# Optimization experiments

Hardware: AMD Instinct MI355X
Metric: run time of the kernel (lower is better)

## Reference

```python
import jax, jax.numpy as jnp
import numpy as np

T, D, E, K = 8192, 7168, 256, 8
G, LG = 8, 4  # n_expert_groups, n_limited_groups
ROUTE_SCALE = 2.5


def setup_inputs() -> dict:
    key = jax.random.key(0)
    k1, k2, k3 = jax.random.split(key, 3)
    x = jax.random.normal(k1, (T, D), dtype=jnp.float32)
    W = jax.random.normal(k2, (E, D), dtype=jnp.float32) * (1.0 / np.sqrt(D))
    bias = jax.random.normal(k3, (E,), dtype=jnp.float32) * 0.01
    return {"x": x, "W": W, "bias": bias}


def reference(x, W, bias):
    # linear scorer: [T, E]
    logits = jnp.einsum("td,ed->te", x, W)
    original_scores = jax.nn.sigmoid(logits)
    scores = original_scores + bias  # bias only affects routing, not weights

    # group selection: reshape [T, G, E//G]; group score = sum of top-2 (bias path)
    scores_g = scores.reshape(T, G, E // G)
    group_scores = jax.lax.top_k(scores_g, 2)[0].sum(axis=-1)  # [T, G]
    _, gidx = jax.lax.top_k(group_scores, LG)  # [T, LG]
    keep = jnp.any(jnp.arange(G)[None, None, :] == gidx[:, :, None], axis=1)  # [T, G]
    scores_masked = jnp.where(keep[:, :, None], scores_g, -jnp.inf).reshape(T, E)

    # final top-k experts
    _, indices = jax.lax.top_k(scores_masked, K)  # [T, K] int32
    weights = jnp.take_along_axis(original_scores, indices, axis=1)  # [T, K]
    weights = weights / weights.sum(axis=-1, keepdims=True)  # sigmoid normalization
    weights = weights * ROUTE_SCALE
    weights = weights.astype(x.dtype)

    # per-expert token counts (indices unique per row, so scatter(1)+sum == histogram)
    counts = jnp.zeros((E,), dtype=jnp.int32).at[indices.reshape(-1)].add(1)
    return weights, indices.astype(jnp.int64), counts
```

## Files before the change

kernel.cpp:

```cpp
#include <hip/hip_runtime.h>
#include <math.h>
#include <stdint.h>

#define T_TOK 8192
#define D_DIM 7168
#define E_EXP 256
#define K_SEL 8
#define G_GRP 8
#define LG_GRP 4
#define ROUTE_SCALE 2.5f

#define BM 64
#define BN 128
#define BK 64
#define NKT (D_DIM / BK)
#define KT_HALF (NKT / 2)
#define SCALE_LO 2048.0f
#define INV_SCALE (1.0f / 2048.0f)

typedef _Float16 half_t;
typedef _Float16 half8 __attribute__((ext_vector_type(8)));
typedef float f32x4 __attribute__((ext_vector_type(4)));

#define WF_HALVES_PER_H (2 * 112 * 16 * 512)

__device__ __forceinline__ void load_lds16(const void* g, void* l) {
    __builtin_amdgcn_global_load_lds(
        (const __attribute__((address_space(1))) uint32_t*)g,
        (__attribute__((address_space(3))) uint32_t*)l, 16, 0, 0);
}

__global__ __launch_bounds__(256)
void convert_W_kernel(const float* __restrict__ W, half_t* __restrict__ Wf) {
    const int u = blockIdx.x * 256 + threadIdx.x;
    const int slot = u & 63;
    const int ks   = (u >> 6) & 1;
    const int p    = (u >> 7) & 7;
    const int t2   = u >> 10;
    const int kt   = t2 % 112;
    const int nb   = t2 / 112;
    const int e = nb * 128 + p * 16 + (slot & 15);
    const int k = kt * 64 + ks * 32 + (slot >> 4) * 8;

    const float* src = W + (size_t)e * D_DIM + k;
    float4 v0 = *(const float4*)src;
    float4 v1 = *(const float4*)(src + 4);
    float f[8] = {v0.x, v0.y, v0.z, v0.w, v1.x, v1.y, v1.z, v1.w};
    half8 hi, lo;
    #pragma unroll
    for (int j = 0; j < 8; j++) {
        const half_t h = (half_t)f[j];
        hi[j] = h;
        lo[j] = (half_t)((f[j] - (float)h) * SCALE_LO);
    }
    *(half8*)&Wf[(size_t)u * 8] = hi;
    *(half8*)&Wf[(size_t)WF_HALVES_PER_H + (size_t)u * 8] = lo;
}

__global__ __launch_bounds__(256, 2)
void gemm_logits_f16split(const float* __restrict__ x,
                          const half_t* __restrict__ Wf,
                          float* __restrict__ plane0,
                          float* __restrict__ plane1) {
    __shared__ __align__(16) half_t Ah[4 * 2 * 64 * 8];
    __shared__ __align__(16) half_t Al[4 * 2 * 64 * 8];
    __shared__ __align__(16) half_t Bbuf[2][32][512];

    const int tid = threadIdx.x;
    const int bid = blockIdx.x;
    const int nb    = bid & 1;
    const int split = (bid >> 1) & 1;
    const int m_blk = bid >> 2;
    const int row0 = m_blk * BM;
    const int ks0  = split * KT_HALF;

    const float* __restrict__ xA = x + (size_t)row0 * D_DIM;
    float* __restrict__ plane = split ? plane1 : plane0;

    const int wave = tid >> 6, lane = tid & 63;
    const int q = lane >> 4;
    const int mp0 = (wave >> 1) * 2;
    const int np0 = (wave & 1) * 4;

    float4 pa[2][2];

    auto load_A = [&](int kt) {
        const int kbase = kt * BK;
        #pragma unroll
        for (int i = 0; i < 2; i++) {
            const int u = i * 256 + tid;
            const int r = u >> 3, k8 = u & 7;
            const float* p = xA + (size_t)r * D_DIM + kbase + k8 * 8;
            pa[i][0] = *(const float4*)p;
            pa[i][1] = *(const float4*)(p + 4);
        }
    };

    auto stage_A = [&]() {
        #pragma unroll
        for (int i = 0; i < 2; i++) {
            const int u = i * 256 + tid;
            const int r = u >> 3, k8 = u & 7;
            float f[8] = {pa[i][0].x, pa[i][0].y, pa[i][0].z, pa[i][0].w,
                          pa[i][1].x, pa[i][1].y, pa[i][1].z, pa[i][1].w};
            half8 hi, lo;
            #pragma unroll
            for (int j = 0; j < 8; j++) {
                const half_t h = (half_t)f[j];
                hi[j] = h;
                lo[j] = (half_t)((f[j] - (float)h) * SCALE_LO);
            }
            const int m = r & 15, qq = k8 & 3, kss = k8 >> 2;
            const int slot = (m + 16 * qq) ^ k8;
            const int off = (((r >> 4) * 2 + kss) * 64 + slot) * 8;
            *(half8*)&Ah[off] = hi;
            *(half8*)&Al[off] = lo;
        }
    };

    auto issue_B = [&](int tt) {
        const int kt = ks0 + tt;
        half_t* bb = &Bbuf[tt & 1][0][0];
        #pragma unroll
        for (int i = 0; i < 8; i++) {
            const int s32 = i * 4 + wave;
            const int h = s32 >> 4, sl = s32 & 15;
            const half_t* src = Wf +
                ((size_t)((h * 2 + nb) * 112 + kt) * 16 + sl) * 512 + lane * 8;
            load_lds16(src, bb + s32 * 512);
        }
    };

    f32x4 ach[2][4] = {}, acc[2][4] = {};

    auto compute = [&](int tt) {
        const half_t* bb = &Bbuf[tt & 1][0][0];
        #pragma unroll
        for (int ks = 0; ks < 2; ks++) {
            const int slot = lane ^ ((ks << 2) | q);
            half8 ah[2], al[2], bh[4], bl[4];
            #pragma unroll
            for (int mi = 0; mi < 2; mi++) {
                const int off = (((mp0 + mi) * 2 + ks) * 64 + slot) * 8;
                ah[mi] = *(const half8*)&Ah[off];
                al[mi] = *(const half8*)&Al[off];
            }
            #pragma unroll
            for (int ni = 0; ni < 4; ni++) {
                const int s32 = (np0 + ni) * 2 + ks;
                bh[ni] = *(const half8*)&bb[s32 * 512 + lane * 8];
                bl[ni] = *(const half8*)&bb[(16 + s32) * 512 + lane * 8];
            }
            #pragma unroll
            for (int mi = 0; mi < 2; mi++)
                #pragma unroll
                for (int ni = 0; ni < 4; ni++) {
                    ach[mi][ni] = __builtin_amdgcn_mfma_f32_16x16x32_f16(ah[mi], bh[ni], ach[mi][ni], 0, 0, 0);
                    acc[mi][ni] = __builtin_amdgcn_mfma_f32_16x16x32_f16(ah[mi], bl[ni], acc[mi][ni], 0, 0, 0);
                    acc[mi][ni] = __builtin_amdgcn_mfma_f32_16x16x32_f16(al[mi], bh[ni], acc[mi][ni], 0, 0, 0);
                }
        }
    };

    issue_B(0);
    load_A(ks0);

    #pragma unroll 1
    for (int tt = 0; tt < KT_HALF; tt++) {
        __syncthreads();
        stage_A();
        __syncthreads();
        if (tt + 1 < KT_HALF) {
            issue_B(tt + 1);
            load_A(ks0 + tt + 1);
        }
        compute(tt);
    }

    const int col0 = nb * BN;
    #pragma unroll
    for (int mi = 0; mi < 2; mi++)
        #pragma unroll
        for (int ni = 0; ni < 4; ni++) {
            const f32x4 vh = ach[mi][ni];
            const f32x4 vc = acc[mi][ni];
            const int ex = col0 + (np0 + ni) * 16 + (lane & 15);
            #pragma unroll
            for (int r = 0; r < 4; r++) {
                const int tok = row0 + (mp0 + mi) * 16 + q * 4 + r;
                plane[(size_t)tok * E_EXP + ex] = vh[r] + vc[r] * INV_SCALE;
            }
        }
}

__global__ __launch_bounds__(256)
void routing_kernel(const float* __restrict__ plane0,
                    const float* __restrict__ plane1,
                    const float* __restrict__ bias,
                    float* __restrict__ out_w,
                    float* __restrict__ out_i) {
    const int wave = threadIdx.x >> 6;
    const int lane = threadIdx.x & 63;
    const int t    = blockIdx.x * 4 + wave;

    const float4 l0 = *(const float4*)(plane0 + (size_t)t * E_EXP + lane * 4);
    const float4 l1 = *(const float4*)(plane1 + (size_t)t * E_EXP + lane * 4);
    const float4 bi = *(const float4*)(bias + lane * 4);
    float lg[4] = {l0.x + l1.x, l0.y + l1.y, l0.z + l1.z, l0.w + l1.w};

    float orig[4], s[4];
    #pragma unroll
    for (int j = 0; j < 4; j++)
        orig[j] = 1.0f / (1.0f + expf(-lg[j]));
    s[0] = orig[0] + bi.x; s[1] = orig[1] + bi.y;
    s[2] = orig[2] + bi.z; s[3] = orig[3] + bi.w;

    float p1 = fmaxf(s[0], s[1]), p2 = fminf(s[0], s[1]);
    float q1 = fmaxf(s[2], s[3]), q2 = fminf(s[2], s[3]);
    float m1 = fmaxf(p1, q1);
    float m2 = fmaxf(fminf(p1, q1), (p1 >= q1) ? p2 : q2);

    #pragma unroll
    for (int off = 1; off <= 4; off <<= 1) {
        float o1 = __shfl_xor(m1, off);
        float o2 = __shfl_xor(m2, off);
        float M1 = fmaxf(m1, o1);
        float M2 = fmaxf(fminf(m1, o1), (m1 >= o1) ? m2 : o2);
        m1 = M1; m2 = M2;
    }
    const float gscore = m1 + m2;

    const int g = lane >> 3;
    int cnt = 0;
    #pragma unroll
    for (int j = 0; j < G_GRP; j++) {
        float gj = __shfl(gscore, j * 8);
        cnt += (gj > gscore || (gj == gscore && j < g)) ? 1 : 0;
    }
    const bool keep = (cnt < LG_GRP);

    float smask[4];
    #pragma unroll
    for (int j = 0; j < 4; j++) smask[j] = keep ? s[j] : -INFINITY;

    float wsum = 0.0f, my_o = 0.0f;
    int my_i = 0;

    #pragma unroll
    for (int k = 0; k < K_SEL; k++) {
        float bv = smask[0]; float bo = orig[0]; int bs = 0;
        if (smask[1] > bv) { bv = smask[1]; bo = orig[1]; bs = 1; }
        if (smask[2] > bv) { bv = smask[2]; bo = orig[2]; bs = 2; }
        if (smask[3] > bv) { bv = smask[3]; bo = orig[3]; bs = 3; }
        int bidx = lane * 4 + bs;

        #pragma unroll
        for (int off = 32; off >= 1; off >>= 1) {
            float ov = __shfl_xor(bv, off);
            float oo = __shfl_xor(bo, off);
            int   oi = __shfl_xor(bidx, off);
            if (ov > bv || (ov == bv && oi < bidx)) { bv = ov; bo = oo; bidx = oi; }
        }
        wsum += bo;
        if (lane == k) { my_o = bo; my_i = bidx; }
        if ((bidx >> 2) == lane) {
            const int sl = bidx & 3;
            smask[0] = (sl == 0) ? -INFINITY : smask[0];
            smask[1] = (sl == 1) ? -INFINITY : smask[1];
            smask[2] = (sl == 2) ? -INFINITY : smask[2];
            smask[3] = (sl == 3) ? -INFINITY : smask[3];
        }
    }

    if (lane < K_SEL) {
        out_w[(size_t)t * K_SEL + lane] = my_o * ROUTE_SCALE / wsum;
        out_i[(size_t)t * K_SEL + lane] = (float)my_i;
    }
}

__global__ __launch_bounds__(256)
void count_kernel(const float* __restrict__ idxf, float* __restrict__ out_c) {
    const float fe = (float)blockIdx.x;
    int c = 0;
    const float4* p = (const float4*)idxf;
    for (int i = threadIdx.x; i < (T_TOK * K_SEL / 4); i += 256) {
        float4 v = p[i];
        c += (v.x == fe) + (v.y == fe) + (v.z == fe) + (v.w == fe);
    }
    __shared__ int red[4];
    #pragma unroll
    for (int off = 32; off >= 1; off >>= 1) c += __shfl_down(c, off);
    if ((threadIdx.x & 63) == 0) red[threadIdx.x >> 6] = c;
    __syncthreads();
    if (threadIdx.x == 0)
        out_c[blockIdx.x] = (float)(red[0] + red[1] + red[2] + red[3]);
}

extern "C" void kernel_launch(void* const* d_in, const int* in_sizes, int n_in,
                              void* d_out, int out_size, void* d_ws, size_t ws_size,
                              hipStream_t stream) {
    const float* x    = (const float*)d_in[0];
    const float* W    = (const float*)d_in[1];
    const float* bias = (const float*)d_in[2];

    float* out   = (float*)d_out;
    float* out_w = out;
    float* out_i = out + (size_t)T_TOK * K_SEL;
    float* out_c = out + (size_t)2 * T_TOK * K_SEL;

    float* plane0 = (float*)d_ws;
    float* plane1 = plane0 + (size_t)T_TOK * E_EXP;
    half_t* Wf    = (half_t*)(plane1 + (size_t)T_TOK * E_EXP);

    hipLaunchKernelGGL(convert_W_kernel, dim3(896), dim3(256), 0, stream, W, Wf);
    hipLaunchKernelGGL(gemm_logits_f16split, dim3(512), dim3(256), 0, stream,
                       x, Wf, plane0, plane1);
    hipLaunchKernelGGL(routing_kernel, dim3(T_TOK / 4), dim3(256), 0, stream,
                       plane0, plane1, bias, out_w, out_i);
    hipLaunchKernelGGL(count_kernel, dim3(E_EXP), dim3(256), 0, stream,
                       out_i, out_c);
}
```

Before: 394.3 us.

## Stage fp32 x tiles directly to LDS via async loads and convert in compute loop

Reworks the logits GEMM. M tile grows from 64 to 128 rows, K step shrinks to 32, and split-K goes from 2 to 4 slices, keeping 512 blocks. A tiles are now copied as raw fp32 straight into LDS with global_load_lds, and the fp16 hi/lo split happens in registers during compute. This removes the register staging pass and one barrier per iteration. The costs are redundant A conversion across the two N-column blocks, double the split-K partial planes for the routing kernel to sum, and more accumulators per wave, which adds register pressure.

```diff
diff --git a/kernel.cpp b/kernel.cpp
--- a/kernel.cpp
+++ b/kernel.cpp
@@ -10,19 +10,16 @@
 #define LG_GRP 4
 #define ROUTE_SCALE 2.5f
 
-#define BM 64
-#define BN 128
-#define BK 64
-#define NKT (D_DIM / BK)
-#define KT_HALF (NKT / 2)
+#define BKT 32
+#define NKT32 (D_DIM / BKT)
+#define SPLITK 4
+#define KT_SLICE (NKT32 / SPLITK)
 #define SCALE_LO 2048.0f
 #define INV_SCALE (1.0f / 2048.0f)
 
 typedef _Float16 half_t;
 typedef _Float16 half8 __attribute__((ext_vector_type(8)));
 typedef float f32x4 __attribute__((ext_vector_type(4)));
-
-#define WF_HALVES_PER_H (2 * 112 * 16 * 512)
 
 __device__ __forceinline__ void load_lds16(const void* g, void* l) {
     __builtin_amdgcn_global_load_lds(
@@ -32,15 +29,14 @@
 
 __global__ __launch_bounds__(256)
 void convert_W_kernel(const float* __restrict__ W, half_t* __restrict__ Wf) {
-    const int u = blockIdx.x * 256 + threadIdx.x;
-    const int slot = u & 63;
-    const int ks   = (u >> 6) & 1;
-    const int p    = (u >> 7) & 7;
-    const int t2   = u >> 10;
-    const int kt   = t2 % 112;
-    const int nb   = t2 / 112;
-    const int e = nb * 128 + p * 16 + (slot & 15);
-    const int k = kt * 64 + ks * 32 + (slot >> 4) * 8;
+    const int v = blockIdx.x * 256 + threadIdx.x;
+    const int slot = v & 63;
+    const int p    = (v >> 6) & 7;
+    const int rest = v >> 9;
+    const int ktg  = rest % NKT32;
+    const int n    = rest / NKT32;
+    const int e = n * 128 + p * 16 + (slot & 15);
+    const int k = ktg * BKT + (slot >> 4) * 8;
 
     const float* src = W + (size_t)e * D_DIM + k;
     float4 v0 = *(const float4*)src;
@@ -53,149 +49,112 @@
         hi[j] = h;
         lo[j] = (half_t)((f[j] - (float)h) * SCALE_LO);
     }
-    *(half8*)&Wf[(size_t)u * 8] = hi;
-    *(half8*)&Wf[(size_t)WF_HALVES_PER_H + (size_t)u * 8] = lo;
+    half_t* tile = Wf + ((size_t)(n * NKT32 + ktg)) * 8192;
+    *(half8*)&tile[(p * 2 + 0) * 512 + slot * 8] = hi;
+    *(half8*)&tile[(p * 2 + 1) * 512 + slot * 8] = lo;
 }
 
 __global__ __launch_bounds__(256, 2)
 void gemm_logits_f16split(const float* __restrict__ x,
                           const half_t* __restrict__ Wf,
-                          float* __restrict__ plane0,
-                          float* __restrict__ plane1) {
-    __shared__ __align__(16) half_t Ah[4 * 2 * 64 * 8];
-    __shared__ __align__(16) half_t Al[4 * 2 * 64 * 8];
-    __shared__ __align__(16) half_t Bbuf[2][32][512];
+                          float* __restrict__ planes) {
+    __shared__ __align__(16) float  Abuf[2][4096];
+    __shared__ __align__(16) half_t Bbuf[2][8192];
 
     const int tid = threadIdx.x;
     const int bid = blockIdx.x;
-    const int nb    = bid & 1;
-    const int split = (bid >> 1) & 1;
-    const int m_blk = bid >> 2;
-    const int row0 = m_blk * BM;
-    const int ks0  = split * KT_HALF;
+    const int n    = bid & 1;
+    const int sp   = (bid >> 1) & 3;
+    const int mb   = bid >> 3;
+    const int row0 = mb * 128;
+    const int kt0  = sp * KT_SLICE;
 
     const float* __restrict__ xA = x + (size_t)row0 * D_DIM;
-    float* __restrict__ plane = split ? plane1 : plane0;
+    float* __restrict__ plane = planes + (size_t)sp * T_TOK * E_EXP;
 
     const int wave = tid >> 6, lane = tid & 63;
+    const int wm = wave >> 1, wn = wave & 1;
+    const int np0 = wn * 4;
     const int q = lane >> 4;
-    const int mp0 = (wave >> 1) * 2;
-    const int np0 = (wave & 1) * 4;
-
-    float4 pa[2][2];
-
-    auto load_A = [&](int kt) {
-        const int kbase = kt * BK;
-        #pragma unroll
-        for (int i = 0; i < 2; i++) {
-            const int u = i * 256 + tid;
-            const int r = u >> 3, k8 = u & 7;
-            const float* p = xA + (size_t)r * D_DIM + kbase + k8 * 8;
-            pa[i][0] = *(const float4*)p;
-            pa[i][1] = *(const float4*)(p + 4);
+
+    auto issue = [&](int t) {
+        const int ktg = kt0 + t;
+        const int b = t & 1;
+        #pragma unroll
+        for (int i = 0; i < 4; i++) {
+            const int sa = wave * 4 + i;
+            const int p = sa >> 1, r = sa & 1;
+            const float* src = xA + (size_t)(p * 16 + (lane & 15)) * D_DIM
+                             + ktg * BKT + q * 8 + r * 4;
+            load_lds16(src, &Abuf[b][sa * 256]);
+        }
+        const half_t* tile = Wf + ((size_t)(n * NKT32 + ktg)) * 8192;
+        #pragma unroll
+        for (int i = 0; i < 4; i++) {
+            const int sb = wave * 4 + i;
+            load_lds16(tile + sb * 512 + lane * 8, &Bbuf[b][sb * 512]);
         }
     };
 
-    auto stage_A = [&]() {
-        #pragma unroll
-        for (int i = 0; i < 2; i++) {
-            const int u = i * 256 + tid;
-            const int r = u >> 3, k8 = u & 7;
-            float f[8] = {pa[i][0].x, pa[i][0].y, pa[i][0].z, pa[i][0].w,
-                          pa[i][1].x, pa[i][1].y, pa[i][1].z, pa[i][1].w};
-            half8 hi, lo;
+    f32x4 ach[4][4] = {}, acx[4][4] = {};
+
+    auto compute = [&](int t) {
+        const int b = t & 1;
+        half8 bh[4], bl[4];
+        #pragma unroll
+        for (int ni = 0; ni < 4; ni++) {
+            const int p = np0 + ni;
+            bh[ni] = *(const half8*)&Bbuf[b][(p * 2 + 0) * 512 + lane * 8];
+            bl[ni] = *(const half8*)&Bbuf[b][(p * 2 + 1) * 512 + lane * 8];
+        }
+        half8 ah[4], al[4];
+        #pragma unroll
+        for (int mi = 0; mi < 4; mi++) {
+            const int p = wm * 4 + mi;
+            const float4 f0 = *(const float4*)&Abuf[b][((p * 2 + 0) * 64 + lane) * 4];
+            const float4 f1 = *(const float4*)&Abuf[b][((p * 2 + 1) * 64 + lane) * 4];
+            const float f[8] = {f0.x, f0.y, f0.z, f0.w, f1.x, f1.y, f1.z, f1.w};
             #pragma unroll
             for (int j = 0; j < 8; j++) {
                 const half_t h = (half_t)f[j];
-                hi[j] = h;
-                lo[j] = (half_t)((f[j] - (float)h) * SCALE_LO);
+                ah[mi][j] = h;
+                al[mi][j] = (half_t)((f[j] - (float)h) * SCALE_LO);
             }
-            const int m = r & 15, qq = k8 & 3, kss = k8 >> 2;
-            const int slot = (m + 16 * qq) ^ k8;
-            const int off = (((r >> 4) * 2 + kss) * 64 + slot) * 8;
-            *(half8*)&Ah[off] = hi;
-            *(half8*)&Al[off] = lo;
-        }
-    };
-
-    auto issue_B = [&](int tt) {
-        const int kt = ks0 + tt;
-        half_t* bb = &Bbuf[tt & 1][0][0];
-        #pragma unroll
-        for (int i = 0; i < 8; i++) {
-            const int s32 = i * 4 + wave;
-            const int h = s32 >> 4, sl = s32 & 15;
-            const half_t* src = Wf +
-                ((size_t)((h * 2 + nb) * 112 + kt) * 16 + sl) * 512 + lane * 8;
-            load_lds16(src, bb + s32 * 512);
-        }
-    };
-
-    f32x4 ach[2][4] = {}, acc[2][4] = {};
-
-    auto compute = [&](int tt) {
-        const half_t* bb = &Bbuf[tt & 1][0][0];
-        #pragma unroll
-        for (int ks = 0; ks < 2; ks++) {
-            const int slot = lane ^ ((ks << 2) | q);
-            half8 ah[2], al[2], bh[4], bl[4];
-            #pragma unroll
-            for (int mi = 0; mi < 2; mi++) {
-                const int off = (((mp0 + mi) * 2 + ks) * 64 + slot) * 8;
-                ah[mi] = *(const half8*)&Ah[off];
-                al[mi] = *(const half8*)&Al[off];
-            }
+        }
+        #pragma unroll
+        for (int mi = 0; mi < 4; mi++)
             #pragma unroll
             for (int ni = 0; ni < 4; ni++) {
-                const int s32 = (np0 + ni) * 2 + ks;
-                bh[ni] = *(const half8*)&bb[s32 * 512 + lane * 8];
-                bl[ni] = *(const half8*)&bb[(16 + s32) * 512 + lane * 8];
+                ach[mi][ni] = __builtin_amdgcn_mfma_f32_16x16x32_f16(ah[mi], bh[ni], ach[mi][ni], 0, 0, 0);
+                acx[mi][ni] = __builtin_amdgcn_mfma_f32_16x16x32_f16(ah[mi], bl[ni], acx[mi][ni], 0, 0, 0);
+                acx[mi][ni] = __builtin_amdgcn_mfma_f32_16x16x32_f16(al[mi], bh[ni], acx[mi][ni], 0, 0, 0);
             }
-            #pragma unroll
-            for (int mi = 0; mi < 2; mi++)
-                #pragma unroll
-                for (int ni = 0; ni < 4; ni++) {
-                    ach[mi][ni] = __builtin_amdgcn_mfma_f32_16x16x32_f16(ah[mi], bh[ni], ach[mi][ni], 0, 0, 0);
-                    acc[mi][ni] = __builtin_amdgcn_mfma_f32_16x16x32_f16(ah[mi], bl[ni], acc[mi][ni], 0, 0, 0);
-                    acc[mi][ni] = __builtin_amdgcn_mfma_f32_16x16x32_f16(al[mi], bh[ni], acc[mi][ni], 0, 0, 0);
-                }
-        }
     };
 
-    issue_B(0);
-    load_A(ks0);
-
+    issue(0);
     #pragma unroll 1
-    for (int tt = 0; tt < KT_HALF; tt++) {
+    for (int t = 0; t < KT_SLICE; t++) {
         __syncthreads();
-        stage_A();
-        __syncthreads();
-        if (tt + 1 < KT_HALF) {
-            issue_B(tt + 1);
-            load_A(ks0 + tt + 1);
-        }
-        compute(tt);
-    }
-
-    const int col0 = nb * BN;
-    #pragma unroll
-    for (int mi = 0; mi < 2; mi++)
+        if (t + 1 < KT_SLICE) issue(t + 1);
+        compute(t);
+    }
+
+    #pragma unroll
+    for (int mi = 0; mi < 4; mi++)
         #pragma unroll
         for (int ni = 0; ni < 4; ni++) {
-            const f32x4 vh = ach[mi][ni];
-            const f32x4 vc = acc[mi][ni];
-            const int ex = col0 + (np0 + ni) * 16 + (lane & 15);
+            const int ex = n * 128 + (np0 + ni) * 16 + (lane & 15);
             #pragma unroll
             for (int r = 0; r < 4; r++) {
-                const int tok = row0 + (mp0 + mi) * 16 + q * 4 + r;
-                plane[(size_t)tok * E_EXP + ex] = vh[r] + vc[r] * INV_SCALE;
+                const int tok = row0 + (wm * 4 + mi) * 16 + q * 4 + r;
+                plane[(size_t)tok * E_EXP + ex] =
+                    ach[mi][ni][r] + acx[mi][ni][r] * INV_SCALE;
             }
         }
 }
 
 __global__ __launch_bounds__(256)
-void routing_kernel(const float* __restrict__ plane0,
-                    const float* __restrict__ plane1,
+void routing_kernel(const float* __restrict__ planes,
                     const float* __restrict__ bias,
                     float* __restrict__ out_w,
                     float* __restrict__ out_i) {
@@ -203,10 +162,14 @@
     const int lane = threadIdx.x & 63;
     const int t    = blockIdx.x * 4 + wave;
 
-    const float4 l0 = *(const float4*)(plane0 + (size_t)t * E_EXP + lane * 4);
-    const float4 l1 = *(const float4*)(plane1 + (size_t)t * E_EXP + lane * 4);
+    float lg[4] = {0.f, 0.f, 0.f, 0.f};
+    #pragma unroll
+    for (int spp = 0; spp < SPLITK; spp++) {
+        const float4 l = *(const float4*)(planes + (size_t)spp * T_TOK * E_EXP
+                                          + (size_t)t * E_EXP + lane * 4);
+        lg[0] += l.x; lg[1] += l.y; lg[2] += l.z; lg[3] += l.w;
+    }
     const float4 bi = *(const float4*)(bias + lane * 4);
-    float lg[4] = {l0.x + l1.x, l0.y + l1.y, l0.z + l1.z, l0.w + l1.w};
 
     float orig[4], s[4];
     #pragma unroll
@@ -308,15 +271,14 @@
     float* out_i = out + (size_t)T_TOK * K_SEL;
     float* out_c = out + (size_t)2 * T_TOK * K_SEL;
 
-    float* plane0 = (float*)d_ws;
-    float* plane1 = plane0 + (size_t)T_TOK * E_EXP;
-    half_t* Wf    = (half_t*)(plane1 + (size_t)T_TOK * E_EXP);
+    float* planes = (float*)d_ws;
+    half_t* Wf = (half_t*)(planes + (size_t)SPLITK * T_TOK * E_EXP);
 
     hipLaunchKernelGGL(convert_W_kernel, dim3(896), dim3(256), 0, stream, W, Wf);
     hipLaunchKernelGGL(gemm_logits_f16split, dim3(512), dim3(256), 0, stream,
-                       x, Wf, plane0, plane1);
+                       x, Wf, planes);
     hipLaunchKernelGGL(routing_kernel, dim3(T_TOK / 4), dim3(256), 0, stream,
-                       plane0, plane1, bias, out_w, out_i);
+                       planes, bias, out_w, out_i);
     hipLaunchKernelGGL(count_kernel, dim3(E_EXP), dim3(256), 0, stream,
                        out_i, out_c);
 }
```

Measured after the change: 410.7 us. 1.04x slower.
